# Kernel tuning notes

Measured on AMD Instinct MI355X. Metric: run time of the kernel, lower is better.

Reference implementation:

```python
import jax, jax.numpy as jnp
import numpy as np

S, D, H = 8192, 2048, 2048


def setup_inputs() -> dict:
    key = jax.random.key(0)
    k1, k2, k3, k4, k5 = jax.random.split(key, 5)
    scale = 1.0 / np.sqrt(H)
    x = jax.random.normal(k1, (S, D), dtype=jnp.float32)
    W_ih = jax.random.uniform(k2, (3 * H, D), minval=-scale, maxval=scale, dtype=jnp.float32)
    W_hh = jax.random.uniform(k3, (3 * H, H), minval=-scale, maxval=scale, dtype=jnp.float32)
    b_ih = jax.random.uniform(k4, (3 * H,), minval=-scale, maxval=scale, dtype=jnp.float32)
    b_hh = jax.random.uniform(k5, (3 * H,), minval=-scale, maxval=scale, dtype=jnp.float32)
    return {"x": x, "W_ih": W_ih, "W_hh": W_hh, "b_ih": b_ih, "b_hh": b_hh}


def reference(x, W_ih, W_hh, b_ih, b_hh):
    # PyTorch nn.GRU, single layer, batch=1, returns final hidden state [1,1,H].
    h_dim = W_hh.shape[1]
    # One big GEMM for all input projections: [S, 3H]
    xi = x @ W_ih.T + b_ih

    def step(h, xt):
        gh = h @ W_hh.T + b_hh              # [3H]
        xr, xz, xn = jnp.split(xt, 3)
        hr, hz, hn = jnp.split(gh, 3)
        r = jax.nn.sigmoid(xr + hr)
        z = jax.nn.sigmoid(xz + hz)
        n = jnp.tanh(xn + r * hn)
        h_new = (1.0 - z) * n + z * h
        return h_new, None

    h0 = jnp.zeros((h_dim,), dtype=x.dtype)
    h_final, _ = jax.lax.scan(step, h0, xi)
    return h_final.reshape(1, 1, h_dim)
```

## Files before the change

### kernel.cpp

```cpp
#include <hip/hip_runtime.h>
#include <hip/hip_fp16.h>

static constexpr int kH   = 2048;
static constexpr int kS   = 8192;
static constexpr int kNWG = 256;
static constexpr int kTHR = 512;

typedef float        v2f __attribute__((ext_vector_type(2)));
typedef unsigned int v4u __attribute__((ext_vector_type(4)));

__device__ __forceinline__ v2f unpk_bf(unsigned int u) {
    union { unsigned int i; float f; } lo, hi;
    lo.i = u << 16; hi.i = u & 0xffff0000u;
    v2f r; r[0] = lo.f; r[1] = hi.f; return r;
}
__device__ __forceinline__ unsigned int pkbf(float lo, float hi) {
    union { float f; unsigned int u; } a, b; a.f = lo; b.f = hi;
    unsigned int ar = a.u + 0x7fffu + ((a.u >> 16) & 1u);
    unsigned int br = b.u + 0x7fffu + ((b.u >> 16) & 1u);
    return (ar >> 16) | (br & 0xffff0000u);
}
__device__ __forceinline__ v2f cvt2h(unsigned int u) {
    __half2 h = *(__half2*)&u;
    float2 f = __half22float2(h);
    v2f r; r[0] = f.x; r[1] = f.y; return r;
}

__device__ __forceinline__ void poll4(const void* p, v4u& a, v4u& b, v4u& c, v4u& d) {
    asm volatile("global_load_dwordx4 %0, %4, off sc0 sc1\n\t"
                 "global_load_dwordx4 %1, %4, off offset:1024 sc0 sc1\n\t"
                 "global_load_dwordx4 %2, %4, off offset:2048 sc0 sc1\n\t"
                 "global_load_dwordx4 %3, %4, off offset:3072 sc0 sc1\n\t"
                 "s_waitcnt vmcnt(0)"
                 : "=&v"(a), "=&v"(b), "=&v"(c), "=&v"(d) : "v"(p) : "memory");
}
__device__ __forceinline__ void store16_coh(void* p, v4u v) {
    asm volatile("global_store_dwordx4 %0, %1, off sc0 sc1"
                 :: "v"(p), "v"(v) : "memory");
}

#define DPP_ADD(v, ctrl)                                                      \
    v += __int_as_float(__builtin_amdgcn_update_dpp(                          \
        0, __float_as_int(v), (ctrl), 0xf, 0xf, true))
#define RED_STAGE(ctrl) do { DPP_ADD(pr, ctrl); DPP_ADD(pz, ctrl);            \
                             DPP_ADD(pxn, ctrl); DPP_ADD(phn, ctrl); } while (0)

__global__ __launch_bounds__(kTHR, 2)
void gru_persistent(const float* __restrict__ x,
                    const float* __restrict__ Wih,
                    const float* __restrict__ Whh,
                    const float* __restrict__ bih,
                    const float* __restrict__ bhh,
                    float* __restrict__ out,
                    unsigned char* __restrict__ rec)
{
    __shared__ __align__(16) unsigned short hlds[kH];
    __shared__ __align__(16) unsigned short hpub[8];

    const int wg  = blockIdx.x;
    const int tid = threadIdx.x;
    const int wv  = tid >> 6;
    const int l   = tid & 63;
    const int e   = wg * 8 + wv;
    const int cb  = 4 * l;
    const int hb  = 8 * l;

    v2f   whh2[3][4][4];
    uint2 wihp[3][8];
#pragma unroll
    for (int G = 0; G < 3; ++G) {
        const size_t row = (size_t)(G * kH + e) * kH;
#pragma unroll
        for (int m = 0; m < 4; ++m) {
            const size_t off = row + hb + 512 * m;
            const float4 w0 = *(const float4*)(Whh + off);
            const float4 w1 = *(const float4*)(Whh + off + 4);
            whh2[G][m][0][0] = w0.x; whh2[G][m][0][1] = w0.y;
            whh2[G][m][1][0] = w0.z; whh2[G][m][1][1] = w0.w;
            whh2[G][m][2][0] = w1.x; whh2[G][m][2][1] = w1.y;
            whh2[G][m][3][0] = w1.z; whh2[G][m][3][1] = w1.w;
        }
#pragma unroll
        for (int m = 0; m < 8; ++m) {
            const float4 iw = *(const float4*)(Wih + row + cb + 256 * m);
            wihp[G][m].x = pkbf(iw.x, iw.y);
            wihp[G][m].y = pkbf(iw.z, iw.w);
        }
    }
    const float bir  = bih[e];
    const float biz  = bih[kH + e];
    const float bin_ = bih[2 * kH + e];
    const float bhr  = bhh[e];
    const float bhz  = bhh[kH + e];
    const float bhn  = bhh[2 * kH + e];

    float hold = 0.0f;

#pragma unroll 1
    for (int t = 0; t < kS; ++t) {
        const float* xrow = x + (size_t)t * kH;
        v2f ar = {0.f, 0.f}, az = {0.f, 0.f}, an = {0.f, 0.f};
#pragma unroll
        for (int m = 0; m < 8; ++m) {
            const float4 xv = *(const float4*)(xrow + cb + 256 * m);
            v2f x0; x0[0] = xv.x; x0[1] = xv.y;
            v2f x1; x1[0] = xv.z; x1[1] = xv.w;
            ar += unpk_bf(wihp[0][m].x) * x0 + unpk_bf(wihp[0][m].y) * x1;
            az += unpk_bf(wihp[1][m].x) * x0 + unpk_bf(wihp[1][m].y) * x1;
            an += unpk_bf(wihp[2][m].x) * x0 + unpk_bf(wihp[2][m].y) * x1;
        }

        if (tid < 64) {
            const unsigned int tg = (unsigned int)(((t >> 1) ^ t) & 1);
            const char* base = (const char*)rec + (t & 1) * 4096 + tid * 16;
            v4u r0, r1, r2, r3;
            for (;;) {
                poll4(base, r0, r1, r2, r3);
                const int ok = ((r0.x & 1u) == tg) & ((r1.x & 1u) == tg) &
                               ((r2.x & 1u) == tg) & ((r3.x & 1u) == tg);
                if (__all(ok)) break;
            }
            *(v4u*)&hlds[tid * 8]         = r0;
            *(v4u*)&hlds[(tid + 64) * 8]  = r1;
            *(v4u*)&hlds[(tid + 128) * 8] = r2;
            *(v4u*)&hlds[(tid + 192) * 8] = r3;
        }
        __syncthreads();

        v2f hr = {0.f, 0.f}, hz = {0.f, 0.f}, hn = {0.f, 0.f};
#pragma unroll
        for (int m = 0; m < 4; ++m) {
            const v4u hu = *(const v4u*)&hlds[hb + 512 * m];
            const v2f h0 = cvt2h(hu.x);
            const v2f h1 = cvt2h(hu.y);
            const v2f h2 = cvt2h(hu.z);
            const v2f h3 = cvt2h(hu.w);
            hr += whh2[0][m][0] * h0 + whh2[0][m][1] * h1 +
                  whh2[0][m][2] * h2 + whh2[0][m][3] * h3;
            hz += whh2[1][m][0] * h0 + whh2[1][m][1] * h1 +
                  whh2[1][m][2] * h2 + whh2[1][m][3] * h3;
            hn += whh2[2][m][0] * h0 + whh2[2][m][1] * h1 +
                  whh2[2][m][2] * h2 + whh2[2][m][3] * h3;
        }

        float pr  = ar[0] + ar[1] + hr[0] + hr[1];
        float pz  = az[0] + az[1] + hz[0] + hz[1];
        float pxn = an[0] + an[1];
        float phn = hn[0] + hn[1];
        RED_STAGE(0xB1);
        RED_STAGE(0x4E);
        RED_STAGE(0x141);
        RED_STAGE(0x140);
        RED_STAGE(0x142);
        RED_STAGE(0x143);

        if (l == 63) {
            const float r = 1.f / (1.f + __expf(-(pr + bir + bhr)));
            const float z = 1.f / (1.f + __expf(-(pz + biz + bhz)));
            const float a = (pxn + bin_) + r * (phn + bhn);
            const float ee = __expf(-2.f * fabsf(a));
            float th = (1.f - ee) / (1.f + ee);
            th = (a < 0.f) ? -th : th;
            hold = (1.f - z) * th + z * hold;
            const __half hh = __float2half(hold);
            hpub[wv] = *(const unsigned short*)&hh;
        }
        __syncthreads();

        if (tid == 0) {
            v4u p = *(const v4u*)hpub;
            const unsigned int tgw = (unsigned int)((((t + 1) >> 1) ^ (t + 1)) & 1);
            p.x = (p.x & ~1u) | tgw;
            store16_coh((char*)rec + ((t + 1) & 1) * 4096 + wg * 16, p);
        }
    }

    if (l == 63)
        out[e] = hold;
}

extern "C" void kernel_launch(void* const* d_in, const int* in_sizes, int n_in,
                              void* d_out, int out_size, void* d_ws, size_t ws_size,
                              hipStream_t stream) {
    (void)in_sizes; (void)n_in; (void)out_size; (void)ws_size;
    const float* x   = (const float*)d_in[0];
    const float* Wih = (const float*)d_in[1];
    const float* Whh = (const float*)d_in[2];
    const float* bih = (const float*)d_in[3];
    const float* bhh = (const float*)d_in[4];

    unsigned char* rec = (unsigned char*)d_ws;
    hipMemsetAsync(rec, 0, 8192, stream);
    gru_persistent<<<dim3(kNWG), dim3(kTHR), 0, stream>>>(
        x, Wih, Whh, bih, bhh, (float*)d_out, rec);
}
```

Measured before the change: 18.16 ms.

## Add dedicated comm wavefront and prefetch next-step input projection

Adds a ninth wavefront per workgroup that only polls the global hidden-state exchange, fills LDS, then waits on per-wave tagged LDS words and publishes the packed half-precision output. Compute waves drop the second barrier per step and compute the next step's input projection right after publishing, so x loading and FMA overlap the cross-workgroup wait. This removes a barrier and pulls work off the critical path. The cost is an extra wave, a looser launch bound that may change register allocation, and LDS spin-waiting.

```diff
diff --git a/kernel.cpp b/kernel.cpp
--- a/kernel.cpp
+++ b/kernel.cpp
@@ -4,7 +4,7 @@
 static constexpr int kH   = 2048;
 static constexpr int kS   = 8192;
 static constexpr int kNWG = 256;
-static constexpr int kTHR = 512;
+static constexpr int kTHR = 576;
 
 typedef float        v2f __attribute__((ext_vector_type(2)));
 typedef unsigned int v4u __attribute__((ext_vector_type(4)));
@@ -45,7 +45,7 @@
 #define RED_STAGE(ctrl) do { DPP_ADD(pr, ctrl); DPP_ADD(pz, ctrl);            \
                              DPP_ADD(pxn, ctrl); DPP_ADD(phn, ctrl); } while (0)
 
-__global__ __launch_bounds__(kTHR, 2)
+__global__ __launch_bounds__(kTHR)
 void gru_persistent(const float* __restrict__ x,
                     const float* __restrict__ Wih,
                     const float* __restrict__ Whh,
@@ -55,15 +55,64 @@
                     unsigned char* __restrict__ rec)
 {
     __shared__ __align__(16) unsigned short hlds[kH];
-    __shared__ __align__(16) unsigned short hpub[8];
+    __shared__ __align__(16) unsigned int   hpubd[8];
 
     const int wg  = blockIdx.x;
     const int tid = threadIdx.x;
     const int wv  = tid >> 6;
     const int l   = tid & 63;
-    const int e   = wg * 8 + wv;
-    const int cb  = 4 * l;
-    const int hb  = 8 * l;
+
+    if (tid < 8) hpubd[tid] = 0u;
+    __syncthreads();
+
+    if (wv == 8) {
+        const char* base0 = (const char*)rec + l * 16;
+#pragma unroll 1
+        for (int t = 0; t < kS; ++t) {
+            const unsigned int tg = (unsigned int)(((t >> 1) ^ t) & 1);
+            const char* base = base0 + (t & 1) * 4096;
+            v4u r0, r1, r2, r3;
+            for (;;) {
+                poll4(base, r0, r1, r2, r3);
+                const int ok = ((r0.x & 1u) == tg) & ((r1.x & 1u) == tg) &
+                               ((r2.x & 1u) == tg) & ((r3.x & 1u) == tg);
+                if (__all(ok)) break;
+            }
+            *(v4u*)&hlds[l * 8]         = r0;
+            *(v4u*)&hlds[(l + 64) * 8]  = r1;
+            *(v4u*)&hlds[(l + 128) * 8] = r2;
+            *(v4u*)&hlds[(l + 192) * 8] = r3;
+            __syncthreads();
+
+            if (l == 0) {
+                const unsigned int tagx = ((unsigned int)(t + 1)) << 16;
+                volatile unsigned int* hp = hpubd;
+                unsigned int d0, d1, d2, d3, d4, d5, d6, d7;
+                for (;;) {
+                    d0 = hp[0]; d1 = hp[1]; d2 = hp[2]; d3 = hp[3];
+                    d4 = hp[4]; d5 = hp[5]; d6 = hp[6]; d7 = hp[7];
+                    const unsigned int mis =
+                        (d0 ^ tagx) | (d1 ^ tagx) | (d2 ^ tagx) | (d3 ^ tagx) |
+                        (d4 ^ tagx) | (d5 ^ tagx) | (d6 ^ tagx) | (d7 ^ tagx);
+                    if ((mis & 0xffff0000u) == 0u) break;
+                }
+                v4u p;
+                p.x = (d0 & 0xffffu) | (d1 << 16);
+                p.y = (d2 & 0xffffu) | (d3 << 16);
+                p.z = (d4 & 0xffffu) | (d5 << 16);
+                p.w = (d6 & 0xffffu) | (d7 << 16);
+                const unsigned int tgw =
+                    (unsigned int)((((t + 1) >> 1) ^ (t + 1)) & 1);
+                p.x = (p.x & ~1u) | tgw;
+                store16_coh((char*)rec + ((t + 1) & 1) * 4096 + wg * 16, p);
+            }
+        }
+        return;
+    }
+
+    const int e  = wg * 8 + wv;
+    const int cb = 4 * l;
+    const int hb = 8 * l;
 
     v2f   whh2[3][4][4];
     uint2 wihp[3][8];
@@ -96,38 +145,25 @@
 
     float hold = 0.0f;
 
-#pragma unroll 1
-    for (int t = 0; t < kS; ++t) {
-        const float* xrow = x + (size_t)t * kH;
-        v2f ar = {0.f, 0.f}, az = {0.f, 0.f}, an = {0.f, 0.f};
+    v2f zero2; zero2[0] = 0.f; zero2[1] = 0.f;
+    v2f ar = zero2, az = zero2, an = zero2;
+    {
 #pragma unroll
         for (int m = 0; m < 8; ++m) {
-            const float4 xv = *(const float4*)(xrow + cb + 256 * m);
+            const float4 xv = *(const float4*)(x + cb + 256 * m);
             v2f x0; x0[0] = xv.x; x0[1] = xv.y;
             v2f x1; x1[0] = xv.z; x1[1] = xv.w;
             ar += unpk_bf(wihp[0][m].x) * x0 + unpk_bf(wihp[0][m].y) * x1;
             az += unpk_bf(wihp[1][m].x) * x0 + unpk_bf(wihp[1][m].y) * x1;
             an += unpk_bf(wihp[2][m].x) * x0 + unpk_bf(wihp[2][m].y) * x1;
         }
-
-        if (tid < 64) {
-            const unsigned int tg = (unsigned int)(((t >> 1) ^ t) & 1);
-            const char* base = (const char*)rec + (t & 1) * 4096 + tid * 16;
-            v4u r0, r1, r2, r3;
-            for (;;) {
-                poll4(base, r0, r1, r2, r3);
-                const int ok = ((r0.x & 1u) == tg) & ((r1.x & 1u) == tg) &
-                               ((r2.x & 1u) == tg) & ((r3.x & 1u) == tg);
-                if (__all(ok)) break;
-            }
-            *(v4u*)&hlds[tid * 8]         = r0;
-            *(v4u*)&hlds[(tid + 64) * 8]  = r1;
-            *(v4u*)&hlds[(tid + 128) * 8] = r2;
-            *(v4u*)&hlds[(tid + 192) * 8] = r3;
-        }
+    }
+
+#pragma unroll 1
+    for (int t = 0; t < kS; ++t) {
         __syncthreads();
 
-        v2f hr = {0.f, 0.f}, hz = {0.f, 0.f}, hn = {0.f, 0.f};
+        v2f hr = zero2, hz = zero2, hn = zero2;
 #pragma unroll
         for (int m = 0; m < 4; ++m) {
             const v4u hu = *(const v4u*)&hlds[hb + 512 * m];
@@ -163,15 +199,23 @@
             th = (a < 0.f) ? -th : th;
             hold = (1.f - z) * th + z * hold;
             const __half hh = __float2half(hold);
-            hpub[wv] = *(const unsigned short*)&hh;
-        }
-        __syncthreads();
-
-        if (tid == 0) {
-            v4u p = *(const v4u*)hpub;
-            const unsigned int tgw = (unsigned int)((((t + 1) >> 1) ^ (t + 1)) & 1);
-            p.x = (p.x & ~1u) | tgw;
-            store16_coh((char*)rec + ((t + 1) & 1) * 4096 + wg * 16, p);
+            const unsigned int hs = *(const unsigned short*)&hh;
+            *(volatile unsigned int*)&hpubd[wv] =
+                hs | (((unsigned int)(t + 1)) << 16);
+        }
+
+        {
+            const float* xrow = x + (size_t)(t + 1 < kS ? t + 1 : t) * kH;
+            ar = zero2; az = zero2; an = zero2;
+#pragma unroll
+            for (int m = 0; m < 8; ++m) {
+                const float4 xv = *(const float4*)(xrow + cb + 256 * m);
+                v2f x0; x0[0] = xv.x; x0[1] = xv.y;
+                v2f x1; x1[0] = xv.z; x1[1] = xv.w;
+                ar += unpk_bf(wihp[0][m].x) * x0 + unpk_bf(wihp[0][m].y) * x1;
+                az += unpk_bf(wihp[1][m].x) * x0 + unpk_bf(wihp[1][m].y) * x1;
+                an += unpk_bf(wihp[2][m].x) * x0 + unpk_bf(wihp[2][m].y) * x1;
+            }
         }
     }
 
```

Measured after the change: 72.21 ms. 298% more time.

## Use fp16 dot2 for recurrent matvec and replace barrier with tagged LDS flags

Applied to the files above, without the earlier changes.

Stores W_hh in registers as packed fp16 and computes the recurrent dot products with v_dot2_f32_f16, which halves register use and roughly halves the ALU instructions on the serial critical path. It also removes the second per-step __syncthreads. Each wave now writes its hidden value to LDS together with a step tag, and thread 0 spins until all eight tags match before publishing. This trades a block-wide barrier for LDS polling and lowers W_hh precision to fp16.

```diff
diff --git a/kernel.cpp b/kernel.cpp
--- a/kernel.cpp
+++ b/kernel.cpp
@@ -8,6 +8,7 @@
 
 typedef float        v2f __attribute__((ext_vector_type(2)));
 typedef unsigned int v4u __attribute__((ext_vector_type(4)));
+typedef _Float16     h2  __attribute__((ext_vector_type(2)));
 
 __device__ __forceinline__ v2f unpk_bf(unsigned int u) {
     union { unsigned int i; float f; } lo, hi;
@@ -20,10 +21,8 @@
     unsigned int br = b.u + 0x7fffu + ((b.u >> 16) & 1u);
     return (ar >> 16) | (br & 0xffff0000u);
 }
-__device__ __forceinline__ v2f cvt2h(unsigned int u) {
-    __half2 h = *(__half2*)&u;
-    float2 f = __half22float2(h);
-    v2f r; r[0] = f.x; r[1] = f.y; return r;
+__device__ __forceinline__ h2 as_h2(unsigned int u) {
+    union { unsigned int i; h2 h; } c; c.i = u; return c.h;
 }
 
 __device__ __forceinline__ void poll4(const void* p, v4u& a, v4u& b, v4u& c, v4u& d) {
@@ -55,7 +54,7 @@
                     unsigned char* __restrict__ rec)
 {
     __shared__ __align__(16) unsigned short hlds[kH];
-    __shared__ __align__(16) unsigned short hpub[8];
+    __shared__ __align__(16) unsigned int   hpubd[8];
 
     const int wg  = blockIdx.x;
     const int tid = threadIdx.x;
@@ -65,7 +64,10 @@
     const int cb  = 4 * l;
     const int hb  = 8 * l;
 
-    v2f   whh2[3][4][4];
+    if (tid < 8) hpubd[tid] = 0u;
+    __syncthreads();
+
+    h2    whhh[3][4][4];
     uint2 wihp[3][8];
 #pragma unroll
     for (int G = 0; G < 3; ++G) {
@@ -75,10 +77,12 @@
             const size_t off = row + hb + 512 * m;
             const float4 w0 = *(const float4*)(Whh + off);
             const float4 w1 = *(const float4*)(Whh + off + 4);
-            whh2[G][m][0][0] = w0.x; whh2[G][m][0][1] = w0.y;
-            whh2[G][m][1][0] = w0.z; whh2[G][m][1][1] = w0.w;
-            whh2[G][m][2][0] = w1.x; whh2[G][m][2][1] = w1.y;
-            whh2[G][m][3][0] = w1.z; whh2[G][m][3][1] = w1.w;
+            h2 t0; t0[0] = (_Float16)w0.x; t0[1] = (_Float16)w0.y;
+            h2 t1; t1[0] = (_Float16)w0.z; t1[1] = (_Float16)w0.w;
+            h2 t2; t2[0] = (_Float16)w1.x; t2[1] = (_Float16)w1.y;
+            h2 t3; t3[0] = (_Float16)w1.z; t3[1] = (_Float16)w1.w;
+            whhh[G][m][0] = t0; whhh[G][m][1] = t1;
+            whhh[G][m][2] = t2; whhh[G][m][3] = t3;
         }
 #pragma unroll
         for (int m = 0; m < 8; ++m) {
@@ -127,26 +131,32 @@
         }
         __syncthreads();
 
-        v2f hr = {0.f, 0.f}, hz = {0.f, 0.f}, hn = {0.f, 0.f};
+        float hr = 0.f, hz = 0.f, hn = 0.f;
 #pragma unroll
         for (int m = 0; m < 4; ++m) {
             const v4u hu = *(const v4u*)&hlds[hb + 512 * m];
-            const v2f h0 = cvt2h(hu.x);
-            const v2f h1 = cvt2h(hu.y);
-            const v2f h2 = cvt2h(hu.z);
-            const v2f h3 = cvt2h(hu.w);
-            hr += whh2[0][m][0] * h0 + whh2[0][m][1] * h1 +
-                  whh2[0][m][2] * h2 + whh2[0][m][3] * h3;
-            hz += whh2[1][m][0] * h0 + whh2[1][m][1] * h1 +
-                  whh2[1][m][2] * h2 + whh2[1][m][3] * h3;
-            hn += whh2[2][m][0] * h0 + whh2[2][m][1] * h1 +
-                  whh2[2][m][2] * h2 + whh2[2][m][3] * h3;
-        }
-
-        float pr  = ar[0] + ar[1] + hr[0] + hr[1];
-        float pz  = az[0] + az[1] + hz[0] + hz[1];
+            const h2 h0 = as_h2(hu.x);
+            const h2 h1 = as_h2(hu.y);
+            const h2 h2v = as_h2(hu.z);
+            const h2 h3 = as_h2(hu.w);
+            hr = __builtin_amdgcn_fdot2(whhh[0][m][0], h0, hr, false);
+            hz = __builtin_amdgcn_fdot2(whhh[1][m][0], h0, hz, false);
+            hn = __builtin_amdgcn_fdot2(whhh[2][m][0], h0, hn, false);
+            hr = __builtin_amdgcn_fdot2(whhh[0][m][1], h1, hr, false);
+            hz = __builtin_amdgcn_fdot2(whhh[1][m][1], h1, hz, false);
+            hn = __builtin_amdgcn_fdot2(whhh[2][m][1], h1, hn, false);
+            hr = __builtin_amdgcn_fdot2(whhh[0][m][2], h2v, hr, false);
+            hz = __builtin_amdgcn_fdot2(whhh[1][m][2], h2v, hz, false);
+            hn = __builtin_amdgcn_fdot2(whhh[2][m][2], h2v, hn, false);
+            hr = __builtin_amdgcn_fdot2(whhh[0][m][3], h3, hr, false);
+            hz = __builtin_amdgcn_fdot2(whhh[1][m][3], h3, hz, false);
+            hn = __builtin_amdgcn_fdot2(whhh[2][m][3], h3, hn, false);
+        }
+
+        float pr  = ar[0] + ar[1] + hr;
+        float pz  = az[0] + az[1] + hz;
         float pxn = an[0] + an[1];
-        float phn = hn[0] + hn[1];
+        float phn = hn;
         RED_STAGE(0xB1);
         RED_STAGE(0x4E);
         RED_STAGE(0x141);
@@ -163,12 +173,28 @@
             th = (a < 0.f) ? -th : th;
             hold = (1.f - z) * th + z * hold;
             const __half hh = __float2half(hold);
-            hpub[wv] = *(const unsigned short*)&hh;
-        }
-        __syncthreads();
+            const unsigned int hs = *(const unsigned short*)&hh;
+            *(volatile unsigned int*)&hpubd[wv] =
+                hs | (((unsigned int)(t + 1)) << 16);
+        }
 
         if (tid == 0) {
-            v4u p = *(const v4u*)hpub;
+            const unsigned int tagx = ((unsigned int)(t + 1)) << 16;
+            volatile unsigned int* hp = hpubd;
+            unsigned int d0, d1, d2, d3, d4, d5, d6, d7;
+            for (;;) {
+                d0 = hp[0]; d1 = hp[1]; d2 = hp[2]; d3 = hp[3];
+                d4 = hp[4]; d5 = hp[5]; d6 = hp[6]; d7 = hp[7];
+                const unsigned int mis =
+                    (d0 ^ tagx) | (d1 ^ tagx) | (d2 ^ tagx) | (d3 ^ tagx) |
+                    (d4 ^ tagx) | (d5 ^ tagx) | (d6 ^ tagx) | (d7 ^ tagx);
+                if ((mis & 0xffff0000u) == 0u) break;
+            }
+            v4u p;
+            p.x = (d0 & 0xffffu) | (d1 << 16);
+            p.y = (d2 & 0xffffu) | (d3 << 16);
+            p.z = (d4 & 0xffffu) | (d5 << 16);
+            p.w = (d6 & 0xffffu) | (d7 << 16);
             const unsigned int tgw = (unsigned int)((((t + 1) >> 1) ^ (t + 1)) & 1);
             p.x = (p.x & ~1u) | tgw;
             store16_coh((char*)rec + ((t + 1) & 1) * 4096 + wg * 16, p);
```

After: 24.64 ms. +35.7%, slower.
